# Kernel tuning notes

Hardware: AMD Instinct MI355X
Metric: run time of the kernel (lower is better)

The kernel has to match this reference:

```python
import jax, jax.numpy as jnp
import numpy as np

B, T, D, N = 32, 2048, 1024, 1024  # batch, time, feature dim, n_dense


def setup_inputs() -> dict:
    key = jax.random.key(0)
    ks = jax.random.split(key, 8)
    s = 1.0 / np.sqrt(D)
    return {
        "query": jax.random.normal(ks[0], (B, D), jnp.float32),
        "values": jax.random.normal(ks[1], (B, T, D), jnp.float32),
        "W1": jax.random.uniform(ks[2], (D, N), jnp.float32, -s, s),
        "b1": jnp.zeros((N,), jnp.float32),
        "W2": jax.random.uniform(ks[3], (D, N), jnp.float32, -s, s),
        "b2": jnp.zeros((N,), jnp.float32),
        "V": jax.random.uniform(ks[4], (N, 1), jnp.float32, -1.0 / np.sqrt(N), 1.0 / np.sqrt(N)),
        "bV": jnp.zeros((1,), jnp.float32),
    }


def reference(query, values, W1, b1, W2, b2, V, bV):
    # q_proj: [B, 1, N], v_proj: [B, T, N]
    q_proj = (query @ W1 + b1)[:, None, :]
    v_proj = jnp.einsum("btd,dn->btn", values, W2) + b2
    # score: [B, T, 1]
    score = jnp.tanh(q_proj + v_proj) @ V + bV
    attention_weights = jax.nn.softmax(score, axis=1)  # softmax over time
    # context: [B, D]
    context_vector = jnp.sum(attention_weights * values, axis=1)
    return (context_vector, attention_weights)
```

## Files before the change

kernel.cpp:

```cpp
#include <hip/hip_runtime.h>
#include <hip/hip_bf16.h>

#define B_ 32
#define T_ 2048
#define D_ 1024
#define N_ 1024
#define M_ (B_*T_)

#define BM 64
#define BN 128
#define BK 64
#define NTSPLIT 2
#define NTP (N_ / BN / NTSPLIT)

typedef short bf16x8 __attribute__((ext_vector_type(8)));
typedef float f32x4 __attribute__((ext_vector_type(4)));
typedef unsigned short us4 __attribute__((ext_vector_type(4)));

__device__ __forceinline__ unsigned short bf16_rn(float x) {
    unsigned u = __float_as_uint(x);
    u += 0x7FFFu + ((u >> 16) & 1u);
    return (unsigned short)(u >> 16);
}

__device__ __forceinline__ void gload_lds16(const void* g, void* l) {
    __builtin_amdgcn_global_load_lds(
        (__attribute__((address_space(1))) void*)(g),
        (__attribute__((address_space(3))) void*)(l), 16, 0, 0);
}

__global__ void k_prep(const float* __restrict__ values, unsigned short* __restrict__ Av,
                       const float* __restrict__ W2, unsigned short* __restrict__ Th,
                       const float* __restrict__ query, const float* __restrict__ W1,
                       const float* __restrict__ b1, float* __restrict__ qp) {
    __shared__ float tile[32][33];
    const int blk = blockIdx.x;
    const int tid = threadIdx.x;

    if (blk < 2048) {
        size_t base = (size_t)blk * 32768 + (size_t)tid * 8;
        #pragma unroll 4
        for (int it = 0; it < 16; ++it) {
            size_t i = base + (size_t)it * 2048;
            float4 a = *(const float4*)(values + i);
            float4 b = *(const float4*)(values + i + 4);
            us4 h0, h1;
            h0[0] = bf16_rn(a.x); h0[1] = bf16_rn(a.y);
            h0[2] = bf16_rn(a.z); h0[3] = bf16_rn(a.w);
            h1[0] = bf16_rn(b.x); h1[1] = bf16_rn(b.y);
            h1[2] = bf16_rn(b.z); h1[3] = bf16_rn(b.w);
            *(us4*)(Av + i) = h0;
            *(us4*)(Av + i + 4) = h1;
        }
    } else if (blk < 3072) {
        int t = blk - 2048;
        int n0 = (t & 31) * 32, d0 = (t >> 5) * 32;
        int tx = tid & 31, ty = tid >> 5;
        #pragma unroll
        for (int i = 0; i < 4; i++) {
            int d = d0 + ty + i * 8;
            tile[ty + i * 8][tx] = W2[d * N_ + n0 + tx];
        }
        __syncthreads();
        #pragma unroll
        for (int i = 0; i < 4; i++) {
            int n = n0 + ty + i * 8;
            Th[n * D_ + d0 + tx] = bf16_rn(tile[tx][ty + i * 8]);
        }
    } else {
        int t = blk - 3072;
        int b = t & 31;
        int n = (t >> 5) * 256 + tid;
        const float* q = query + b * D_;
        const float* w = W1 + n;
        float s = 0.f;
        #pragma unroll 8
        for (int d = 0; d < D_; d++) s += q[d] * w[d * N_];
        qp[b * N_ + n] = s + b1[n];
    }
}

__global__ __launch_bounds__(256, 2) void k2_score(
    const unsigned short* __restrict__ Av,
    const unsigned short* __restrict__ W2Th,
    const float* __restrict__ qp,
    const float* __restrict__ b2,
    const float* __restrict__ V,
    float* __restrict__ scorep) {
    __shared__ unsigned short sAh[BM * BK];
    __shared__ unsigned short sBh[BN * BK];
    __shared__ float red[2 * BM];

    const int tid = threadIdx.x;
    const int lane = tid & 63;
    const int wid = tid >> 6;
    const int wm = wid >> 1, wn = wid & 1;
    const int g = lane >> 4, c16 = lane & 15;

    const int bid = blockIdx.x;
    const int wgid = ((bid & 7) << 8) | (bid >> 3);
    const int m0 = (wgid >> 1) * BM;
    const int b = m0 >> 11;
    const int half = wgid & 1;
    const int nt0 = half * NTP;

    const int b_rl = lane >> 3;
    const int b_j = lane & 7;

    float rowpart[8];
    #pragma unroll
    for (int i = 0; i < 8; i++) rowpart[i] = 0.f;

    for (int nt = nt0; nt < nt0 + NTP; nt++) {
        f32x4 acc[2][4];
        #pragma unroll
        for (int mi = 0; mi < 2; mi++)
            #pragma unroll
            for (int ni = 0; ni < 4; ni++) {
                f32x4 z = {0.f, 0.f, 0.f, 0.f};
                acc[mi][ni] = z;
            }

        for (int kt = 0; kt < D_ / BK; kt++) {
            const int k0 = kt * BK;
            __syncthreads();

            #pragma unroll
            for (int i = 0; i < 4; i++) {
                int r = wid * 32 + i * 8 + b_rl;
                int jj = b_j ^ (r & 7);
                size_t soff = (size_t)(nt * BN + r) * D_ + k0 + jj * 8;
                gload_lds16(W2Th + soff, &sBh[(wid * 32 + i * 8) * 64]);
            }
            #pragma unroll
            for (int i = 0; i < 2; i++) {
                int r = wid * 16 + i * 8 + b_rl;
                int jj = b_j ^ (r & 7);
                size_t soff = (size_t)(m0 + r) * D_ + k0 + jj * 8;
                gload_lds16(Av + soff, &sAh[(wid * 16 + i * 8) * 64]);
            }

            __syncthreads();

            #pragma unroll
            for (int s = 0; s < 2; s++) {
                bf16x8 aH[2], bH[4];
                #pragma unroll
                for (int mi = 0; mi < 2; mi++) {
                    int r = wm * 32 + mi * 16 + c16;
                    int idx = r * 64 + (((s * 4 + g) ^ (r & 7)) << 3);
                    aH[mi] = *(const bf16x8*)&sAh[idx];
                }
                #pragma unroll
                for (int ni = 0; ni < 4; ni++) {
                    int r = wn * 64 + ni * 16 + c16;
                    int idx = r * 64 + (((s * 4 + g) ^ (r & 7)) << 3);
                    bH[ni] = *(const bf16x8*)&sBh[idx];
                }
                #pragma unroll
                for (int mi = 0; mi < 2; mi++)
                    #pragma unroll
                    for (int ni = 0; ni < 4; ni++)
                        acc[mi][ni] = __builtin_amdgcn_mfma_f32_16x16x32_bf16(aH[mi], bH[ni], acc[mi][ni], 0, 0, 0);
            }
        }

        #pragma unroll
        for (int ni = 0; ni < 4; ni++) {
            int n = nt * BN + wn * 64 + ni * 16 + c16;
            float qv = qp[b * N_ + n] + b2[n];
            float Vv = V[n];
            #pragma unroll
            for (int mi = 0; mi < 2; mi++)
                #pragma unroll
                for (int r = 0; r < 4; r++) {
                    rowpart[mi * 4 + r] += tanhf(acc[mi][ni][r] + qv) * Vv;
                }
        }
    }

    #pragma unroll
    for (int i = 0; i < 8; i++) {
        float v = rowpart[i];
        v += __shfl_xor(v, 1);
        v += __shfl_xor(v, 2);
        v += __shfl_xor(v, 4);
        v += __shfl_xor(v, 8);
        rowpart[i] = v;
    }
    if (c16 == 0) {
        #pragma unroll
        for (int mi = 0; mi < 2; mi++)
            #pragma unroll
            for (int r = 0; r < 4; r++)
                red[wn * BM + wm * 32 + mi * 16 + g * 4 + r] = rowpart[mi * 4 + r];
    }
    __syncthreads();
    if (tid < BM) {
        scorep[(size_t)half * M_ + m0 + tid] = red[tid] + red[BM + tid];
    }
}

__global__ void k3_softmax(const float* __restrict__ sp,
                           float* __restrict__ sw) {
    int b = blockIdx.x;
    const float* r0 = sp + b * T_;
    const float* r1 = sp + M_ + b * T_;
    float* row = sw + b * T_;
    int tid = threadIdx.x;
    float v[8];
    float lmax = -1e30f;
    #pragma unroll
    for (int i = 0; i < 8; i++) {
        int idx = tid + i * 256;
        v[i] = r0[idx] + r1[idx];
        lmax = fmaxf(lmax, v[i]);
    }
    #pragma unroll
    for (int d = 1; d < 64; d <<= 1) lmax = fmaxf(lmax, __shfl_xor(lmax, d));
    __shared__ float sm[4], ss[4];
    if ((tid & 63) == 0) sm[tid >> 6] = lmax;
    __syncthreads();
    lmax = fmaxf(fmaxf(sm[0], sm[1]), fmaxf(sm[2], sm[3]));
    float lsum = 0.f;
    #pragma unroll
    for (int i = 0; i < 8; i++) {
        v[i] = expf(v[i] - lmax);
        lsum += v[i];
    }
    #pragma unroll
    for (int d = 1; d < 64; d <<= 1) lsum += __shfl_xor(lsum, d);
    if ((tid & 63) == 0) ss[tid >> 6] = lsum;
    __syncthreads();
    lsum = ss[0] + ss[1] + ss[2] + ss[3];
    float inv = 1.f / lsum;
    #pragma unroll
    for (int i = 0; i < 8; i++) row[tid + i * 256] = v[i] * inv;
}

__global__ void k4_context(const unsigned short* __restrict__ Av,
                           const float* __restrict__ w,
                           float* __restrict__ ctx) {
    int b = blockIdx.x;
    int dc = blockIdx.y;
    int tc = blockIdx.z;
    int d4 = threadIdx.x & 31;
    int th = threadIdx.x >> 5;
    const float* wrow = w + b * T_;
    int d = dc * 128 + d4 * 4;
    const unsigned short* vbase = Av + (size_t)b * T_ * D_ + d;
    float4 acc = {0.f, 0.f, 0.f, 0.f};
    int t0 = tc * 256 + th * 32;
    for (int t = t0; t < t0 + 32; t++) {
        float wt = wrow[t];
        us4 hv = *(const us4*)(vbase + (size_t)t * D_);
        acc.x += wt * __uint_as_float((unsigned)hv[0] << 16);
        acc.y += wt * __uint_as_float((unsigned)hv[1] << 16);
        acc.z += wt * __uint_as_float((unsigned)hv[2] << 16);
        acc.w += wt * __uint_as_float((unsigned)hv[3] << 16);
    }
    __shared__ float4 red4[256];
    red4[threadIdx.x] = acc;
    __syncthreads();
    if (th == 0) {
        float4 s = red4[d4];
        #pragma unroll
        for (int i = 1; i < 8; i++) {
            float4 o = red4[i * 32 + d4];
            s.x += o.x; s.y += o.y; s.z += o.z; s.w += o.w;
        }
        atomicAdd(&ctx[b * D_ + d + 0], s.x);
        atomicAdd(&ctx[b * D_ + d + 1], s.y);
        atomicAdd(&ctx[b * D_ + d + 2], s.z);
        atomicAdd(&ctx[b * D_ + d + 3], s.w);
    }
}

extern "C" void kernel_launch(void* const* d_in, const int* in_sizes, int n_in,
                              void* d_out, int out_size, void* d_ws, size_t ws_size,
                              hipStream_t stream) {
    const float* query  = (const float*)d_in[0];
    const float* values = (const float*)d_in[1];
    const float* W1     = (const float*)d_in[2];
    const float* b1     = (const float*)d_in[3];
    const float* W2     = (const float*)d_in[4];
    const float* b2     = (const float*)d_in[5];
    const float* V      = (const float*)d_in[6];

    float* ctx = (float*)d_out;
    float* weights = (float*)d_out + B_ * D_;

    size_t need = (size_t)N_ * D_ * sizeof(unsigned short)
                + (size_t)B_ * N_ * sizeof(float)
                + (size_t)NTSPLIT * M_ * sizeof(float)
                + (size_t)M_ * D_ * sizeof(unsigned short);
    if (ws_size < need) return;
    unsigned short* Th = (unsigned short*)d_ws;
    float* qp = (float*)(Th + (size_t)N_ * D_);
    float* scorep = qp + (size_t)B_ * N_;
    unsigned short* Av = (unsigned short*)(scorep + (size_t)NTSPLIT * M_);

    k_prep<<<3200, 256, 0, stream>>>(values, Av, W2, Th, query, W1, b1, qp);
    k2_score<<<(M_ / BM) * NTSPLIT, 256, 0, stream>>>(Av, Th, qp, b2, V, scorep);
    k3_softmax<<<B_, 256, 0, stream>>>(scorep, weights);
    hipMemsetAsync(ctx, 0, (size_t)B_ * D_ * sizeof(float), stream);
    k4_context<<<dim3(B_, 8, 8), 256, 0, stream>>>(Av, weights, ctx);
}
```

Before: 347.0 us.

## Fuse values bf16 conversion into score GEMM and zero ctx in softmax

```diff
diff --git a/kernel.cpp b/kernel.cpp
--- a/kernel.cpp
+++ b/kernel.cpp
@@ -29,32 +29,15 @@
         (__attribute__((address_space(3))) void*)(l), 16, 0, 0);
 }
 
-__global__ void k_prep(const float* __restrict__ values, unsigned short* __restrict__ Av,
-                       const float* __restrict__ W2, unsigned short* __restrict__ Th,
+__global__ void k_prep(const float* __restrict__ W2, unsigned short* __restrict__ Th,
                        const float* __restrict__ query, const float* __restrict__ W1,
                        const float* __restrict__ b1, float* __restrict__ qp) {
     __shared__ float tile[32][33];
     const int blk = blockIdx.x;
     const int tid = threadIdx.x;
 
-    if (blk < 2048) {
-        size_t base = (size_t)blk * 32768 + (size_t)tid * 8;
-        #pragma unroll 4
-        for (int it = 0; it < 16; ++it) {
-            size_t i = base + (size_t)it * 2048;
-            float4 a = *(const float4*)(values + i);
-            float4 b = *(const float4*)(values + i + 4);
-            us4 h0, h1;
-            h0[0] = bf16_rn(a.x); h0[1] = bf16_rn(a.y);
-            h0[2] = bf16_rn(a.z); h0[3] = bf16_rn(a.w);
-            h1[0] = bf16_rn(b.x); h1[1] = bf16_rn(b.y);
-            h1[2] = bf16_rn(b.z); h1[3] = bf16_rn(b.w);
-            *(us4*)(Av + i) = h0;
-            *(us4*)(Av + i + 4) = h1;
-        }
-    } else if (blk < 3072) {
-        int t = blk - 2048;
-        int n0 = (t & 31) * 32, d0 = (t >> 5) * 32;
+    if (blk < 1024) {
+        int n0 = (blk & 31) * 32, d0 = (blk >> 5) * 32;
         int tx = tid & 31, ty = tid >> 5;
         #pragma unroll
         for (int i = 0; i < 4; i++) {
@@ -68,7 +51,7 @@
             Th[n * D_ + d0 + tx] = bf16_rn(tile[tx][ty + i * 8]);
         }
     } else {
-        int t = blk - 3072;
+        int t = blk - 1024;
         int b = t & 31;
         int n = (t >> 5) * 256 + tid;
         const float* q = query + b * D_;
@@ -81,7 +64,8 @@
 }
 
 __global__ __launch_bounds__(256, 2) void k2_score(
-    const unsigned short* __restrict__ Av,
+    const float* __restrict__ values,
+    unsigned short* __restrict__ Av,
     const unsigned short* __restrict__ W2Th,
     const float* __restrict__ qp,
     const float* __restrict__ b2,
@@ -106,12 +90,15 @@
 
     const int b_rl = lane >> 3;
     const int b_j = lane & 7;
+    const int a_c4 = tid & 15;
+    const int a_r0 = tid >> 4;
 
     float rowpart[8];
     #pragma unroll
     for (int i = 0; i < 8; i++) rowpart[i] = 0.f;
 
-    for (int nt = nt0; nt < nt0 + NTP; nt++) {
+    for (int ip = 0; ip < NTP; ip++) {
+        const int nt = nt0 + ip;
         f32x4 acc[2][4];
         #pragma unroll
         for (int mi = 0; mi < 2; mi++)
@@ -132,12 +119,29 @@
                 size_t soff = (size_t)(nt * BN + r) * D_ + k0 + jj * 8;
                 gload_lds16(W2Th + soff, &sBh[(wid * 32 + i * 8) * 64]);
             }
-            #pragma unroll
-            for (int i = 0; i < 2; i++) {
-                int r = wid * 16 + i * 8 + b_rl;
-                int jj = b_j ^ (r & 7);
-                size_t soff = (size_t)(m0 + r) * D_ + k0 + jj * 8;
-                gload_lds16(Av + soff, &sAh[(wid * 16 + i * 8) * 64]);
+
+            if (ip > 0) {
+                #pragma unroll
+                for (int i = 0; i < 2; i++) {
+                    int r = wid * 16 + i * 8 + b_rl;
+                    int jj = b_j ^ (r & 7);
+                    size_t soff = (size_t)(m0 + r) * D_ + k0 + jj * 8;
+                    gload_lds16(Av + soff, &sAh[(wid * 16 + i * 8) * 64]);
+                }
+            } else {
+                const float* abase = values + (size_t)m0 * D_ + k0;
+                #pragma unroll
+                for (int p = 0; p < 4; p++) {
+                    int r = p * 16 + a_r0;
+                    float4 v = *(const float4*)(abase + (size_t)r * D_ + a_c4 * 4);
+                    us4 hv;
+                    hv[0] = bf16_rn(v.x); hv[1] = bf16_rn(v.y);
+                    hv[2] = bf16_rn(v.z); hv[3] = bf16_rn(v.w);
+                    int idx = r * 64 + ((((a_c4 >> 1) ^ (r & 7)) << 3) | ((a_c4 & 1) << 2));
+                    *(us4*)&sAh[idx] = hv;
+                    size_t goff = (size_t)(m0 + r) * D_ + k0 + a_c4 * 4;
+                    *(us4*)&Av[goff] = hv;
+                }
             }
 
             __syncthreads();
@@ -202,12 +206,17 @@
 }
 
 __global__ void k3_softmax(const float* __restrict__ sp,
-                           float* __restrict__ sw) {
+                           float* __restrict__ sw,
+                           float* __restrict__ ctx) {
     int b = blockIdx.x;
     const float* r0 = sp + b * T_;
     const float* r1 = sp + M_ + b * T_;
     float* row = sw + b * T_;
     int tid = threadIdx.x;
+
+    #pragma unroll
+    for (int i = 0; i < 4; i++) ctx[b * D_ + tid + i * 256] = 0.f;
+
     float v[8];
     float lmax = -1e30f;
     #pragma unroll
@@ -300,9 +309,8 @@
     float* scorep = qp + (size_t)B_ * N_;
     unsigned short* Av = (unsigned short*)(scorep + (size_t)NTSPLIT * M_);
 
-    k_prep<<<3200, 256, 0, stream>>>(values, Av, W2, Th, query, W1, b1, qp);
-    k2_score<<<(M_ / BM) * NTSPLIT, 256, 0, stream>>>(Av, Th, qp, b2, V, scorep);
-    k3_softmax<<<B_, 256, 0, stream>>>(scorep, weights);
-    hipMemsetAsync(ctx, 0, (size_t)B_ * D_ * sizeof(float), stream);
+    k_prep<<<1152, 256, 0, stream>>>(W2, Th, query, W1, b1, qp);
+    k2_score<<<(M_ / BM) * NTSPLIT, 256, 0, stream>>>(values, Av, Th, qp, b2, V, scorep);
+    k3_softmax<<<B_, 256, 0, stream>>>(scorep, weights, ctx);
     k4_context<<<dim3(B_, 8, 8), 256, 0, stream>>>(Av, weights, ctx);
 }
```

After: 369.1 us. 1.06x slower.
